# Optimization experiments

Hardware: AMD Instinct MI355X
Metric: run time of the kernel (lower is better)

Reference implementation:

```python
import jax, jax.numpy as jnp
import numpy as np

B, T, M, D = 2, 2048, 2048, 128
H = M // D
ROTARY_BASE = 10000
NORM_EPS = 1e-6
QK_SCALE = 1.0 / D  # mult = sqrt(qk_scale) applied to both q and k
INFTY_APPROX = 1e30


def setup_inputs() -> dict:
    key = jax.random.key(0)
    ks = jax.random.split(key, 6)
    w_scale = M ** (-0.5)
    return {
        "x": jax.random.normal(ks[0], (B, T, M), jnp.float32),
        "wq": jax.random.normal(ks[1], (M, H, D), jnp.float32) * w_scale,
        "wk": jax.random.normal(ks[2], (M, H, D), jnp.float32) * w_scale,
        "wv": jax.random.normal(ks[3], (M, H, D), jnp.float32) * w_scale,
        "wo": jax.random.normal(ks[4], (H, D, M), jnp.float32) * w_scale,
        "gq": jnp.zeros((H, 1, D), jnp.float32),
        "bq": jnp.zeros((H, 1, D), jnp.float32),
        "gk": jnp.zeros((H, 1, D), jnp.float32),
        "bk": jnp.zeros((H, 1, D), jnp.float32),
    }


def _qk_layernorm(x, g, b):
    # x: [B,H,T,D]; g,b: [H,1,D]; centered RMS norm with trainable (1+g), b
    x = x - jnp.mean(x, axis=-1, keepdims=True)
    x = x / jnp.sqrt(jnp.mean(jnp.square(x), axis=-1, keepdims=True) + NORM_EPS)
    return x * (1.0 + g)[None] + b[None]


def _rotary(x):
    # x: [B,H,T,D]; half-split rotary encoding
    half = D // 2
    positions = jnp.arange(T, dtype=jnp.float32)[:, None]          # [T,1]
    ang_freqs = jnp.power(float(ROTARY_BASE), -jnp.arange(half, dtype=jnp.float32) / half)[None, :]  # [1,half]
    radians = positions * ang_freqs                                  # [T,half]
    cos = jnp.cos(radians)[None, None].astype(x.dtype)               # [1,1,T,half]
    sin = jnp.sin(radians)[None, None].astype(x.dtype)
    even, odd = jnp.split(x, 2, axis=-1)
    return jnp.concatenate([even * cos - odd * sin, even * sin + odd * cos], axis=-1)


def reference(x, wq, wk, wv, wo, gq, bq, gk, bk):
    q = jnp.einsum('bim,mhd->bhid', x, wq)
    k = jnp.einsum('bim,mhd->bhid', x, wk)
    v = jnp.einsum('bim,mhd->bhid', x, wv)
    q = _rotary(_qk_layernorm(q, gq, bq))
    k = _rotary(_qk_layernorm(k, gk, bk))
    mult = jnp.asarray(QK_SCALE ** 0.5, dtype=x.dtype)
    s = jnp.einsum('bhid,bhjd->bhij', q * mult, k * mult)            # [B,H,T,T]
    i = jnp.arange(T)[:, None]
    j = jnp.arange(T)[None, :]
    future = (i < j)[None, None]                                      # mask future positions
    s = s - jnp.asarray(INFTY_APPROX, dtype=s.dtype) * future
    p = jax.nn.softmax(s, axis=-1)
    o = jnp.einsum('bhij,bhjd->bhid', p, v)
    return jnp.einsum('bhid,hdm->bim', o, wo)
```

## Files before the change

kernel.cpp:

```cpp
#include <hip/hip_runtime.h>


#define NB 2
#define NT 2048
#define NM 2048
#define NH 16
#define ND 128

typedef __attribute__((ext_vector_type(4))) float f32x4;
typedef __attribute__((ext_vector_type(8))) short bf16x8;
typedef __attribute__((ext_vector_type(4))) short bf16x4;

#define AS1 __attribute__((address_space(1)))
#define AS3 __attribute__((address_space(3)))

#define SW(r) (((r) ^ ((r) >> 2)) & 3)

__device__ __forceinline__ unsigned short f2bf(float f){
  unsigned int u = __float_as_uint(f);
  u = (u + 0x7fffu + ((u >> 16) & 1u)) >> 16;
  return (unsigned short)u;
}
__device__ __forceinline__ float bf2f(short s){
  return __uint_as_float(((unsigned int)(unsigned short)s) << 16);
}
__device__ __forceinline__ void gload_lds16(const void* g, void* l){
  __builtin_amdgcn_global_load_lds((const AS1 void*)g, (AS3 void*)l, 16, 0, 0);
}

__global__ __launch_bounds__(256) void prep_k(const float* __restrict__ x,
                                              const float* __restrict__ wq,
                                              const float* __restrict__ wk,
                                              const float* __restrict__ wv,
                                              const float* __restrict__ wo,
                                              short* __restrict__ xb,
                                              short* __restrict__ wT,
                                              float* __restrict__ ctab,
                                              float* __restrict__ stab){
  __shared__ float tl[32][33];
  const int bid = blockIdx.x, tid = threadIdx.x;
  if (bid < 8192){
    size_t gid = (size_t)bid * 256 + tid;
    float4 v = *(const float4*)(x + gid * 4);
    bf16x4 o;
    o[0] = (short)f2bf(v.x); o[1] = (short)f2bf(v.y);
    o[2] = (short)f2bf(v.z); o[3] = (short)f2bf(v.w);
    *(bf16x4*)(xb + gid * 4) = o;
  } else if (bid < 24576){
    int tb = bid - 8192;
    int z = tb >> 12, rem = tb & 4095;
    int n0 = (rem & 63) * 32, k0 = (rem >> 6) * 32;
    const float* src = (z == 0) ? wq : (z == 1) ? wk : (z == 2) ? wv : wo;
    short* dst = wT + (size_t)z * 2048 * 2048;
    int cx = tid & 31, ry = tid >> 5;
    #pragma unroll
    for (int p = 0; p < 4; ++p)
      tl[ry + 8 * p][cx] = src[(size_t)(k0 + ry + 8 * p) * 2048 + n0 + cx];
    __syncthreads();
    #pragma unroll
    for (int p = 0; p < 4; ++p)
      dst[(size_t)(n0 + ry + 8 * p) * 2048 + k0 + cx] =
          (short)f2bf(tl[cx][ry + 8 * p]);
  } else {
    int t = (bid - 24576) * 4 + (tid >> 6);
    int i = tid & 63;
    float freq = __expf(-(float)i * (9.210340371976184f / 64.0f));
    float ang = (float)t * freq;
    ctab[t * 64 + i] = cosf(ang);
    stab[t * 64 + i] = sinf(ang);
  }
}

#define NKT2 64
__global__ __launch_bounds__(512, 4) void gemm256_k(const short* __restrict__ A,
                                                    const short* __restrict__ Bt,
                                                    short* __restrict__ Cq,
                                                    short* __restrict__ Cn,
                                                    const float* __restrict__ gq,
                                                    const float* __restrict__ bq,
                                                    const float* __restrict__ gk,
                                                    const float* __restrict__ bk,
                                                    const float* __restrict__ ctab,
                                                    const float* __restrict__ stab){
  extern __shared__ char lds[];
  const int tid = threadIdx.x;
  const int wid = tid >> 6, lane = tid & 63;
  const int lrow = lane & 15, g8 = lane >> 4;
  const int wm = wid >> 1, wn = wid & 1;
  const int Kdim = 2048;

  int bid = blockIdx.x;
  int s = (bid & 7) * 96 + (bid >> 3);
  const int bx = s & 15;
  const int by = s >> 4;
  const int m0 = bx * 256, n0 = by * 128;

  const int ar = lane >> 2;
  const int ag = (lane & 3) ^ SW(ar);
  const short* Ab = A  + (size_t)(m0 + wid * 32 + ar) * Kdim + ag * 8;
  const short* Bb = Bt + (size_t)(n0 + wid * 16 + ar) * Kdim + ag * 8;

  f32x4 acc[4][4] = {};

  auto STAGE = [&](int c, int kt){
    #pragma unroll
    for (int i = 0; i < 2; ++i)
      gload_lds16(Ab + (size_t)(i * 16) * Kdim + kt * 32,
                  lds + c * 16384 + wid * 2048 + i * 1024);
    gload_lds16(Bb + kt * 32, lds + 32768 + c * 8192 + wid * 1024);
  };
  auto ldA = [&](int c, int mi) -> bf16x8 {
    int row = wm * 64 + mi * 16 + lrow;
    return *(const bf16x8*)(lds + c * 16384 + row * 64 + ((g8 ^ SW(row)) << 4));
  };
  auto ldB = [&](int c, int ni) -> bf16x8 {
    int row = wn * 64 + ni * 16 + lrow;
    return *(const bf16x8*)(lds + 32768 + c * 8192 + row * 64 + ((g8 ^ SW(row)) << 4));
  };

  STAGE(0, 0);

  for (int kt = 0; kt < NKT2; ++kt){
    const int c = kt & 1;
    asm volatile("s_waitcnt vmcnt(0)" ::: "memory");
    __builtin_amdgcn_s_barrier();
    if (kt + 1 < NKT2) STAGE(c ^ 1, kt + 1);

    bf16x8 af[4], bfv[4];
    #pragma unroll
    for (int mi = 0; mi < 4; ++mi) af[mi] = ldA(c, mi);
    #pragma unroll
    for (int ni = 0; ni < 4; ++ni) bfv[ni] = ldB(c, ni);
    #pragma unroll
    for (int mi = 0; mi < 4; ++mi)
      #pragma unroll
      for (int ni = 0; ni < 4; ++ni)
        acc[mi][ni] = __builtin_amdgcn_mfma_f32_16x16x32_bf16(
            af[mi], bfv[ni], acc[mi][ni], 0, 0, 0);
  }

  const int tsel = by >> 4;
  const int hh = by & 15;
  if (tsel < 2){
    const float* gv = tsel ? gk : gq;
    const float* bv = tsel ? bk : bq;
    float* red = (float*)lds;
    short* xch = (short*)(lds + 4096);
    __syncthreads();
    #pragma unroll
    for (int mi = 0; mi < 4; ++mi)
      #pragma unroll
      for (int r = 0; r < 4; ++r){
        float a0 = acc[mi][0][r], a1 = acc[mi][1][r];
        float a2 = acc[mi][2][r], a3 = acc[mi][3][r];
        float s1 = (a0 + a1) + (a2 + a3);
        float s2 = (a0*a0 + a1*a1) + (a2*a2 + a3*a3);
        #pragma unroll
        for (int off = 1; off < 16; off <<= 1){
          s1 += __shfl_xor(s1, off);
          s2 += __shfl_xor(s2, off);
        }
        if (lrow == 0){
          int row = wm * 64 + mi * 16 + g8 * 4 + r;
          red[row * 4 + wn * 2]     = s1;
          red[row * 4 + wn * 2 + 1] = s2;
        }
      }
    __syncthreads();
    #pragma unroll
    for (int mi = 0; mi < 4; ++mi)
      #pragma unroll
      for (int r = 0; r < 4; ++r){
        int row = wm * 64 + mi * 16 + g8 * 4 + r;
        float s1 = red[row * 4] + red[row * 4 + 2];
        float s2 = red[row * 4 + 1] + red[row * 4 + 3];
        float mean = s1 * (1.0f / 128.0f);
        float var = s2 * (1.0f / 128.0f) - mean * mean;
        float rstd = rsqrtf(var + 1e-6f);
        #pragma unroll
        for (int ni = 0; ni < 4; ++ni){
          int d = wn * 64 + ni * 16 + lrow;
          float n = (acc[mi][ni][r] - mean) * rstd * (1.0f + gv[hh * 128 + d])
                    + bv[hh * 128 + d];
          acc[mi][ni][r] = n;
          xch[row * 136 + d] = (short)f2bf(n);
        }
      }
    __syncthreads();
    const float sgn = wn ? 1.0f : -1.0f;
    const float qsc = tsel ? 1.0f : 0.011271055007f;
    short* dstn = Cn + (size_t)tsel * (NB * NH * NT * ND);
    #pragma unroll
    for (int mi = 0; mi < 4; ++mi)
      #pragma unroll
      for (int r = 0; r < 4; ++r){
        int rowb = m0 + wm * 64 + mi * 16 + g8 * 4 + r;
        int b = rowb >> 11, t = rowb & 2047;
        int row = rowb - m0;
        #pragma unroll
        for (int ni = 0; ni < 4; ++ni){
          int d = wn * 64 + ni * 16 + lrow;
          int dl = ni * 16 + lrow;
          float pv = bf2f(xch[row * 136 + (d ^ 64)]);
          float c = ctab[t * 64 + dl], sn = stab[t * 64 + dl];
          float o = (acc[mi][ni][r] * c + sgn * pv * sn) * qsc;
          dstn[(((size_t)(b * NH + hh)) * NT + t) * ND + d] = (short)f2bf(o);
        }
      }
  } else {
    short* dst = Cq + 2 * (size_t)(NB * NH * NT * ND);
    #pragma unroll
    for (int mi = 0; mi < 4; ++mi){
      int rowb = m0 + wm * 64 + mi * 16 + g8 * 4;
      int b = rowb >> 11, t0 = rowb & 2047;
      int jb = t0 >> 6, toff = t0 & 63;
      #pragma unroll
      for (int ni = 0; ni < 4; ++ni){
        int d = wn * 64 + ni * 16 + lrow;
        f32x4 a = acc[mi][ni];
        bf16x4 w4;
        #pragma unroll
        for (int r = 0; r < 4; ++r) w4[r] = (short)f2bf(a[r]);
        *(bf16x4*)&dst[(((size_t)(b * NH + hh) * 32 + jb) * ND + d) * 64 + toff] = w4;
      }
    }
  }
}

__global__ __launch_bounds__(512, 4) void gemmo_k(const short* __restrict__ A,
                                                  const short* __restrict__ Bt,
                                                  float* __restrict__ Cout){
  extern __shared__ char lds[];
  const int tid = threadIdx.x;
  const int wid = tid >> 6, lane = tid & 63;
  const int lrow = lane & 15, g8 = lane >> 4;
  const int wm = wid >> 1, wn = wid & 1;
  const int Kdim = 2048;

  int bid = blockIdx.x;
  int s = (bid & 7) * 32 + (bid >> 3);
  const int bx = s & 15;
  const int by = s >> 4;
  const int m0 = bx * 256, n0 = by * 128;

  const int ar = lane >> 2;
  const int ag = (lane & 3) ^ SW(ar);
  const short* Ab = A  + (size_t)(m0 + wid * 32 + ar) * Kdim + ag * 8;
  const short* Bb = Bt + (size_t)(n0 + wid * 16 + ar) * Kdim + ag * 8;

  f32x4 acc[4][4] = {};

  auto STAGE = [&](int c, int kt){
    #pragma unroll
    for (int i = 0; i < 2; ++i)
      gload_lds16(Ab + (size_t)(i * 16) * Kdim + kt * 32,
                  lds + c * 16384 + wid * 2048 + i * 1024);
    gload_lds16(Bb + kt * 32, lds + 32768 + c * 8192 + wid * 1024);
  };
  auto ldA = [&](int c, int mi) -> bf16x8 {
    int row = wm * 64 + mi * 16 + lrow;
    return *(const bf16x8*)(lds + c * 16384 + row * 64 + ((g8 ^ SW(row)) << 4));
  };
  auto ldB = [&](int c, int ni) -> bf16x8 {
    int row = wn * 64 + ni * 16 + lrow;
    return *(const bf16x8*)(lds + 32768 + c * 8192 + row * 64 + ((g8 ^ SW(row)) << 4));
  };

  STAGE(0, 0);

  for (int kt = 0; kt < NKT2; ++kt){
    const int c = kt & 1;
    asm volatile("s_waitcnt vmcnt(0)" ::: "memory");
    __builtin_amdgcn_s_barrier();
    if (kt + 1 < NKT2) STAGE(c ^ 1, kt + 1);

    bf16x8 af[4], bfv[4];
    #pragma unroll
    for (int mi = 0; mi < 4; ++mi) af[mi] = ldA(c, mi);
    #pragma unroll
    for (int ni = 0; ni < 4; ++ni) bfv[ni] = ldB(c, ni);
    #pragma unroll
    for (int mi = 0; mi < 4; ++mi)
      #pragma unroll
      for (int ni = 0; ni < 4; ++ni)
        acc[mi][ni] = __builtin_amdgcn_mfma_f32_16x16x32_bf16(
            af[mi], bfv[ni], acc[mi][ni], 0, 0, 0);
  }

  #pragma unroll
  for (int mi = 0; mi < 4; ++mi){
    int rowb = m0 + wm * 64 + mi * 16 + g8 * 4;
    #pragma unroll
    for (int ni = 0; ni < 4; ++ni){
      int col = n0 + wn * 64 + ni * 16 + lrow;
      f32x4 a = acc[mi][ni];
      #pragma unroll
      for (int r = 0; r < 4; ++r)
        Cout[(size_t)(rowb + r) * 2048 + col] = a[r];
    }
  }
}

__global__ __launch_bounds__(512) void attn_k(const short* __restrict__ qn,
                                              const short* __restrict__ kn,
                                              const short* __restrict__ vt,
                                              short* __restrict__ ob){
  extern __shared__ char lds[];
  const int tid = threadIdx.x;
  const int wid = tid >> 6, lane = tid & 63;
  const int lrow = lane & 15, g8 = lane >> 4;
  const int id = blockIdx.x;
  const int qs = id >> 5;
  const int bh = id & 31;
  const int b = bh >> 4, h = bh & 15;
  const size_t base = (size_t)bh * NT * ND;
  char* Pw = lds + 98304 + wid * 2048;

  auto STAGE = [&](int jb){
    const int cb = jb % 3;
    #pragma unroll
    for (int i = 0; i < 2; ++i){
      int r0 = wid * 4 + i * 32;
      int r = r0 + (lane >> 4);
      int g = lane & 15;
      gload_lds16(kn + base + (size_t)(jb * 64 + r) * ND + ((g ^ (r & 7)) << 3),
                  lds + cb * 16384 + r0 * 256);
    }
    #pragma unroll
    for (int i = 0; i < 2; ++i){
      int d0 = wid * 8 + i * 64;
      int d = d0 + (lane >> 3);
      int g = lane & 7;
      gload_lds16(vt + base + (size_t)jb * 8192 + d * 64 + ((g ^ (d & 7)) << 3),
                  lds + 49152 + cb * 16384 + d0 * 128);
    }
  };

  for (int pass = 0; pass < 2; ++pass){
    const int qt = pass ? (15 - qs) : qs;
    const int t0 = qt * 128;
    const int wrow0 = t0 + wid * 16;
    const int tq = wrow0 + lrow;
    bf16x8 qf[4];
    #pragma unroll
    for (int dc = 0; dc < 4; ++dc)
      qf[dc] = *(const bf16x8*)(qn + base + (size_t)tq * ND + dc * 32 + g8 * 8);
    f32x4 O[8] = {};
    float m = -3e38f, lsum = 0.0f;
    const int ntiles = 2 * qt + 2;

    __syncthreads();
    STAGE(0);
    STAGE(1);

    for (int jb = 0; jb < ntiles; ++jb){
      if (jb + 1 < ntiles) asm volatile("s_waitcnt vmcnt(4)" ::: "memory");
      else                 asm volatile("s_waitcnt vmcnt(0)" ::: "memory");
      __builtin_amdgcn_s_barrier();
      if (jb + 2 < ntiles) STAGE(jb + 2);
      const char* Kb = lds + (jb % 3) * 16384;
      const char* Vb = lds + 49152 + (jb % 3) * 16384;

      if (jb * 64 <= wrow0 + 15){
        f32x4 st[4] = {};
        __builtin_amdgcn_s_setprio(1);
        #pragma unroll
        for (int dc = 0; dc < 4; ++dc)
          #pragma unroll
          for (int js = 0; js < 4; ++js){
            int jl = js * 16 + lrow;
            bf16x8 kf = *(const bf16x8*)(Kb + jl * 256 +
                          (((dc * 4 + g8) ^ (jl & 7)) << 4));
            st[js] = __builtin_amdgcn_mfma_f32_16x16x32_bf16(kf, qf[dc], st[js], 0, 0, 0);
          }
        __builtin_amdgcn_s_setprio(0);
        if (jb * 64 + 63 > wrow0){
          #pragma unroll
          for (int js = 0; js < 4; ++js)
            #pragma unroll
            for (int r = 0; r < 4; ++r){
              int j = jb * 64 + js * 16 + g8 * 4 + r;
              if (j > tq) st[js][r] = -3e38f;
            }
        }
        f32x4 m4 = st[0];
        #pragma unroll
        for (int js = 1; js < 4; ++js)
          #pragma unroll
          for (int r = 0; r < 4; ++r) m4[r] = fmaxf(m4[r], st[js][r]);
        float mx = fmaxf(fmaxf(m4[0], m4[1]), fmaxf(m4[2], m4[3]));
        mx = fmaxf(mx, __shfl_xor(mx, 16));
        mx = fmaxf(mx, __shfl_xor(mx, 32));
        if (!__all(mx <= m + 8.0f)){
          float mnew = fmaxf(m, mx);
          float fac = exp2f(m - mnew);
          m = mnew;
          lsum *= fac;
          #pragma unroll
          for (int dcb = 0; dcb < 8; ++dcb) O[dcb] *= fac;
        }
        float ps = 0.0f;
        #pragma unroll
        for (int js = 0; js < 4; ++js){
          float p0 = exp2f(st[js][0] - m);
          float p1 = exp2f(st[js][1] - m);
          float p2 = exp2f(st[js][2] - m);
          float p3 = exp2f(st[js][3] - m);
          ps += (p0 + p1) + (p2 + p3);
          unsigned int lo, hi;
          asm("v_cvt_pk_bf16_f32 %0, %1, %2" : "=v"(lo) : "v"(p0), "v"(p1));
          asm("v_cvt_pk_bf16_f32 %0, %1, %2" : "=v"(hi) : "v"(p2), "v"(p3));
          uint2 w; w.x = lo; w.y = hi;
          *(uint2*)(Pw + lrow * 128 + ((js * 32 + g8 * 8) ^ ((lrow & 7) << 4))) = w;
        }
        ps += __shfl_xor(ps, 16);
        ps += __shfl_xor(ps, 32);
        lsum += ps;
        asm volatile("s_waitcnt lgkmcnt(0)" ::: "memory");
        __builtin_amdgcn_s_setprio(1);
        #pragma unroll
        for (int j32 = 0; j32 < 2; ++j32){
          bf16x8 pf = *(const bf16x8*)(Pw + lrow * 128 +
                        ((j32 * 64 + g8 * 16) ^ ((lrow & 7) << 4)));
          #pragma unroll
          for (int dcb = 0; dcb < 8; ++dcb){
            int d = dcb * 16 + lrow;
            bf16x8 vf = *(const bf16x8*)(Vb + d * 128 +
                          (((j32 * 4 + g8) ^ (d & 7)) << 4));
            O[dcb] = __builtin_amdgcn_mfma_f32_16x16x32_bf16(vf, pf, O[dcb], 0, 0, 0);
          }
        }
        __builtin_amdgcn_s_setprio(0);
      }
    }
    float inv = 1.0f / lsum;
    #pragma unroll
    for (int dcb = 0; dcb < 8; ++dcb){
      bf16x4 w4;
      #pragma unroll
      for (int r = 0; r < 4; ++r) w4[r] = (short)f2bf(O[dcb][r] * inv);
      *(bf16x4*)(ob + ((size_t)(b * NT + tq)) * (NH * ND) + h * ND + dcb * 16 + g8 * 4) = w4;
    }
  }
}

extern "C" void kernel_launch(void* const* d_in, const int* in_sizes, int n_in,
                              void* d_out, int out_size, void* d_ws, size_t ws_size,
                              hipStream_t stream){
  const float* x  = (const float*)d_in[0];
  const float* wq = (const float*)d_in[1];
  const float* wk = (const float*)d_in[2];
  const float* wv = (const float*)d_in[3];
  const float* wo = (const float*)d_in[4];
  const float* gq = (const float*)d_in[5];
  const float* bq = (const float*)d_in[6];
  const float* gk = (const float*)d_in[7];
  const float* bk = (const float*)d_in[8];

  char* ws = (char*)d_ws;
  short* xb   = (short*)(ws);
  short* wT   = (short*)(ws + 16777216);
  short* qkvb = (short*)(ws + 50331648);
  short* qkn  = (short*)(ws + 100663296);
  short* ob   = (short*)(ws + 134217728);
  float* ctab = (float*)(ws + 150994944);
  float* stab = (float*)(ws + 151519232);

  (void)hipFuncSetAttribute((const void*)gemm256_k,
                            hipFuncAttributeMaxDynamicSharedMemorySize, 73728);
  (void)hipFuncSetAttribute((const void*)gemmo_k,
                            hipFuncAttributeMaxDynamicSharedMemorySize, 49152);
  (void)hipFuncSetAttribute((const void*)attn_k,
                            hipFuncAttributeMaxDynamicSharedMemorySize, 114688);

  prep_k<<<dim3(25088), dim3(256), 0, stream>>>(x, wq, wk, wv, wo, xb, wT, ctab, stab);
  gemm256_k<<<dim3(768), dim3(512), 73728, stream>>>(xb, wT, qkvb, qkn,
                                                     gq, bq, gk, bk, ctab, stab);
  attn_k<<<dim3(256), dim3(512), 114688, stream>>>(qkn, qkn + 8388608,
                                                   qkvb + 2 * (size_t)8388608, ob);
  gemmo_k<<<dim3(256), dim3(512), 49152, stream>>>(ob, wT + 3 * (size_t)4194304,
                                                   (float*)d_out);
}
```

Measured before the change: 262.5 us.

## Give each wave full head rows in QKV GEMM to skip LDS norm exchange

The QKV projection GEMM now assigns each of the 8 waves a 32x128 tile (2x8 MFMA blocks) instead of a 64x64 tile. Each wave then holds complete head-dimension rows, so the layernorm reduction and rotary pairing (d with d^64) happen entirely in registers. This removes the LDS reduction buffer, the bf16 exchange buffer and three block barriers, and lowers the dynamic shared memory request. In exchange every wave reads all 8 B fragments per k-step (more LDS traffic on B, less on A), and the rotary partner is now used at full fp32 precision rather than rounded to bf16.

```diff
diff --git a/kernel.cpp b/kernel.cpp
--- a/kernel.cpp
+++ b/kernel.cpp
@@ -74,7 +74,7 @@
 #define NKT2 64
 __global__ __launch_bounds__(512, 4) void gemm256_k(const short* __restrict__ A,
                                                     const short* __restrict__ Bt,
-                                                    short* __restrict__ Cq,
+                                                    short* __restrict__ Cv,
                                                     short* __restrict__ Cn,
                                                     const float* __restrict__ gq,
                                                     const float* __restrict__ bq,
@@ -86,7 +86,6 @@
   const int tid = threadIdx.x;
   const int wid = tid >> 6, lane = tid & 63;
   const int lrow = lane & 15, g8 = lane >> 4;
-  const int wm = wid >> 1, wn = wid & 1;
   const int Kdim = 2048;
 
   int bid = blockIdx.x;
@@ -100,7 +99,7 @@
   const short* Ab = A  + (size_t)(m0 + wid * 32 + ar) * Kdim + ag * 8;
   const short* Bb = Bt + (size_t)(n0 + wid * 16 + ar) * Kdim + ag * 8;
 
-  f32x4 acc[4][4] = {};
+  f32x4 acc[2][8] = {};
 
   auto STAGE = [&](int c, int kt){
     #pragma unroll
@@ -110,11 +109,11 @@
     gload_lds16(Bb + kt * 32, lds + 32768 + c * 8192 + wid * 1024);
   };
   auto ldA = [&](int c, int mi) -> bf16x8 {
-    int row = wm * 64 + mi * 16 + lrow;
+    int row = wid * 32 + mi * 16 + lrow;
     return *(const bf16x8*)(lds + c * 16384 + row * 64 + ((g8 ^ SW(row)) << 4));
   };
   auto ldB = [&](int c, int ni) -> bf16x8 {
-    int row = wn * 64 + ni * 16 + lrow;
+    int row = ni * 16 + lrow;
     return *(const bf16x8*)(lds + 32768 + c * 8192 + row * 64 + ((g8 ^ SW(row)) << 4));
   };
 
@@ -126,15 +125,15 @@
     __builtin_amdgcn_s_barrier();
     if (kt + 1 < NKT2) STAGE(c ^ 1, kt + 1);
 
-    bf16x8 af[4], bfv[4];
-    #pragma unroll
-    for (int mi = 0; mi < 4; ++mi) af[mi] = ldA(c, mi);
-    #pragma unroll
-    for (int ni = 0; ni < 4; ++ni) bfv[ni] = ldB(c, ni);
-    #pragma unroll
-    for (int mi = 0; mi < 4; ++mi)
-      #pragma unroll
-      for (int ni = 0; ni < 4; ++ni)
+    bf16x8 af[2], bfv[8];
+    #pragma unroll
+    for (int mi = 0; mi < 2; ++mi) af[mi] = ldA(c, mi);
+    #pragma unroll
+    for (int ni = 0; ni < 8; ++ni) bfv[ni] = ldB(c, ni);
+    #pragma unroll
+    for (int mi = 0; mi < 2; ++mi)
+      #pragma unroll
+      for (int ni = 0; ni < 8; ++ni)
         acc[mi][ni] = __builtin_amdgcn_mfma_f32_16x16x32_bf16(
             af[mi], bfv[ni], acc[mi][ni], 0, 0, 0);
   }
@@ -144,84 +143,64 @@
   if (tsel < 2){
     const float* gv = tsel ? gk : gq;
     const float* bv = tsel ? bk : bq;
-    float* red = (float*)lds;
-    short* xch = (short*)(lds + 4096);
-    __syncthreads();
-    #pragma unroll
-    for (int mi = 0; mi < 4; ++mi)
+    float gcoef[8], bcoef[8];
+    #pragma unroll
+    for (int ni = 0; ni < 8; ++ni){
+      int d = ni * 16 + lrow;
+      gcoef[ni] = 1.0f + gv[hh * 128 + d];
+      bcoef[ni] = bv[hh * 128 + d];
+    }
+    const float qsc = tsel ? 1.0f : 0.011271055007f;
+    short* dstn = Cn + (size_t)tsel * (NB * NH * NT * ND);
+    #pragma unroll
+    for (int mi = 0; mi < 2; ++mi)
       #pragma unroll
       for (int r = 0; r < 4; ++r){
-        float a0 = acc[mi][0][r], a1 = acc[mi][1][r];
-        float a2 = acc[mi][2][r], a3 = acc[mi][3][r];
-        float s1 = (a0 + a1) + (a2 + a3);
-        float s2 = (a0*a0 + a1*a1) + (a2*a2 + a3*a3);
+        float s1 = 0.0f, s2 = 0.0f;
+        #pragma unroll
+        for (int ni = 0; ni < 8; ++ni){
+          float v = acc[mi][ni][r];
+          s1 += v; s2 += v * v;
+        }
         #pragma unroll
         for (int off = 1; off < 16; off <<= 1){
           s1 += __shfl_xor(s1, off);
           s2 += __shfl_xor(s2, off);
         }
-        if (lrow == 0){
-          int row = wm * 64 + mi * 16 + g8 * 4 + r;
-          red[row * 4 + wn * 2]     = s1;
-          red[row * 4 + wn * 2 + 1] = s2;
-        }
-      }
-    __syncthreads();
-    #pragma unroll
-    for (int mi = 0; mi < 4; ++mi)
-      #pragma unroll
-      for (int r = 0; r < 4; ++r){
-        int row = wm * 64 + mi * 16 + g8 * 4 + r;
-        float s1 = red[row * 4] + red[row * 4 + 2];
-        float s2 = red[row * 4 + 1] + red[row * 4 + 3];
         float mean = s1 * (1.0f / 128.0f);
         float var = s2 * (1.0f / 128.0f) - mean * mean;
         float rstd = rsqrtf(var + 1e-6f);
-        #pragma unroll
-        for (int ni = 0; ni < 4; ++ni){
-          int d = wn * 64 + ni * 16 + lrow;
-          float n = (acc[mi][ni][r] - mean) * rstd * (1.0f + gv[hh * 128 + d])
-                    + bv[hh * 128 + d];
-          acc[mi][ni][r] = n;
-          xch[row * 136 + d] = (short)f2bf(n);
-        }
-      }
-    __syncthreads();
-    const float sgn = wn ? 1.0f : -1.0f;
-    const float qsc = tsel ? 1.0f : 0.011271055007f;
-    short* dstn = Cn + (size_t)tsel * (NB * NH * NT * ND);
-    #pragma unroll
-    for (int mi = 0; mi < 4; ++mi)
-      #pragma unroll
-      for (int r = 0; r < 4; ++r){
-        int rowb = m0 + wm * 64 + mi * 16 + g8 * 4 + r;
+        float nv[8];
+        #pragma unroll
+        for (int ni = 0; ni < 8; ++ni)
+          nv[ni] = (acc[mi][ni][r] - mean) * rstd * gcoef[ni] + bcoef[ni];
+        int rowb = m0 + wid * 32 + mi * 16 + g8 * 4 + r;
         int b = rowb >> 11, t = rowb & 2047;
-        int row = rowb - m0;
-        #pragma unroll
-        for (int ni = 0; ni < 4; ++ni){
-          int d = wn * 64 + ni * 16 + lrow;
-          int dl = ni * 16 + lrow;
-          float pv = bf2f(xch[row * 136 + (d ^ 64)]);
+        size_t rbase = (((size_t)(b * NH + hh)) * NT + t) * ND;
+        #pragma unroll
+        for (int lo = 0; lo < 4; ++lo){
+          int dl = lo * 16 + lrow;
           float c = ctab[t * 64 + dl], sn = stab[t * 64 + dl];
-          float o = (acc[mi][ni][r] * c + sgn * pv * sn) * qsc;
-          dstn[(((size_t)(b * NH + hh)) * NT + t) * ND + d] = (short)f2bf(o);
+          float oe = (nv[lo] * c - nv[lo + 4] * sn) * qsc;
+          float oo = (nv[lo] * sn + nv[lo + 4] * c) * qsc;
+          dstn[rbase + dl]      = (short)f2bf(oe);
+          dstn[rbase + dl + 64] = (short)f2bf(oo);
         }
       }
   } else {
-    short* dst = Cq + 2 * (size_t)(NB * NH * NT * ND);
-    #pragma unroll
-    for (int mi = 0; mi < 4; ++mi){
-      int rowb = m0 + wm * 64 + mi * 16 + g8 * 4;
+    #pragma unroll
+    for (int mi = 0; mi < 2; ++mi){
+      int rowb = m0 + wid * 32 + mi * 16 + g8 * 4;
       int b = rowb >> 11, t0 = rowb & 2047;
       int jb = t0 >> 6, toff = t0 & 63;
       #pragma unroll
-      for (int ni = 0; ni < 4; ++ni){
-        int d = wn * 64 + ni * 16 + lrow;
+      for (int ni = 0; ni < 8; ++ni){
+        int d = ni * 16 + lrow;
         f32x4 a = acc[mi][ni];
         bf16x4 w4;
         #pragma unroll
         for (int r = 0; r < 4; ++r) w4[r] = (short)f2bf(a[r]);
-        *(bf16x4*)&dst[(((size_t)(b * NH + hh) * 32 + jb) * ND + d) * 64 + toff] = w4;
+        *(bf16x4*)&Cv[(((size_t)(b * NH + hh) * 32 + jb) * ND + d) * 64 + toff] = w4;
       }
     }
   }
@@ -467,14 +446,15 @@
   float* stab = (float*)(ws + 151519232);
 
   (void)hipFuncSetAttribute((const void*)gemm256_k,
-                            hipFuncAttributeMaxDynamicSharedMemorySize, 73728);
+                            hipFuncAttributeMaxDynamicSharedMemorySize, 49152);
   (void)hipFuncSetAttribute((const void*)gemmo_k,
                             hipFuncAttributeMaxDynamicSharedMemorySize, 49152);
   (void)hipFuncSetAttribute((const void*)attn_k,
                             hipFuncAttributeMaxDynamicSharedMemorySize, 114688);
 
   prep_k<<<dim3(25088), dim3(256), 0, stream>>>(x, wq, wk, wv, wo, xb, wT, ctab, stab);
-  gemm256_k<<<dim3(768), dim3(512), 73728, stream>>>(xb, wT, qkvb, qkn,
+  gemm256_k<<<dim3(768), dim3(512), 49152, stream>>>(xb, wT,
+                                                     qkvb + 2 * (size_t)8388608, qkn,
                                                      gq, bq, gk, bk, ctab, stab);
   attn_k<<<dim3(256), dim3(512), 114688, stream>>>(qkn, qkn + 8388608,
                                                    qkvb + 2 * (size_t)8388608, ob);
```

New measurement: 256.9 us (median of 2 runs). 1.02x faster.

## Interleave Q/K weight columns so rotary partner pairs are exchanged via lane shuffle

Applied to the files above, without the earlier changes.

The prep kernel now permutes the Q and K weight columns within each head so that rotary partners d and d+64 land in adjacent columns. The GEMM epilogue can then fetch the partner value with a lane shuffle instead of writing normalized values to LDS, syncing, and reading them back. It also hoists the gain and bias loads into registers and reduces dynamic shared memory, which may raise occupancy. In exchange, q and k are stored in an interleaved dimension order, which is only valid because q·k dot products do not depend on the order of d.

```diff
diff --git a/kernel.cpp b/kernel.cpp
--- a/kernel.cpp
+++ b/kernel.cpp
@@ -58,9 +58,14 @@
       tl[ry + 8 * p][cx] = src[(size_t)(k0 + ry + 8 * p) * 2048 + n0 + cx];
     __syncthreads();
     #pragma unroll
-    for (int p = 0; p < 4; ++p)
-      dst[(size_t)(n0 + ry + 8 * p) * 2048 + k0 + cx] =
-          (short)f2bf(tl[cx][ry + 8 * p]);
+    for (int p = 0; p < 4; ++p){
+      int n = n0 + ry + 8 * p;
+      if (z < 2){
+        int d = n & 127;
+        n = (n & ~127) | (((d & 63) << 1) | (d >> 6));
+      }
+      dst[(size_t)n * 2048 + k0 + cx] = (short)f2bf(tl[cx][ry + 8 * p]);
+    }
   } else {
     int t = (bid - 24576) * 4 + (tid >> 6);
     int i = tid & 63;
@@ -74,7 +79,7 @@
 #define NKT2 64
 __global__ __launch_bounds__(512, 4) void gemm256_k(const short* __restrict__ A,
                                                     const short* __restrict__ Bt,
-                                                    short* __restrict__ Cq,
+                                                    short* __restrict__ Cv,
                                                     short* __restrict__ Cn,
                                                     const float* __restrict__ gq,
                                                     const float* __restrict__ bq,
@@ -145,7 +150,14 @@
     const float* gv = tsel ? gk : gq;
     const float* bv = tsel ? bk : bq;
     float* red = (float*)lds;
-    short* xch = (short*)(lds + 4096);
+    float gcoef[4], bcoef[4];
+    #pragma unroll
+    for (int ni = 0; ni < 4; ++ni){
+      int p = wn * 64 + ni * 16 + lrow;
+      int d = (p >> 1) + ((p & 1) << 6);
+      gcoef[ni] = 1.0f + gv[hh * 128 + d];
+      bcoef[ni] = bv[hh * 128 + d];
+    }
     __syncthreads();
     #pragma unroll
     for (int mi = 0; mi < 4; ++mi)
@@ -167,6 +179,9 @@
         }
       }
     __syncthreads();
+    const float qsc = tsel ? 1.0f : 0.011271055007f;
+    const float sgn = (lrow & 1) ? 1.0f : -1.0f;
+    short* dstn = Cn + (size_t)tsel * (NB * NH * NT * ND);
     #pragma unroll
     for (int mi = 0; mi < 4; ++mi)
       #pragma unroll
@@ -177,38 +192,20 @@
         float mean = s1 * (1.0f / 128.0f);
         float var = s2 * (1.0f / 128.0f) - mean * mean;
         float rstd = rsqrtf(var + 1e-6f);
+        int rowb = m0 + row;
+        int b = rowb >> 11, t = rowb & 2047;
+        size_t rbase = (((size_t)(b * NH + hh)) * NT + t) * ND;
         #pragma unroll
         for (int ni = 0; ni < 4; ++ni){
-          int d = wn * 64 + ni * 16 + lrow;
-          float n = (acc[mi][ni][r] - mean) * rstd * (1.0f + gv[hh * 128 + d])
-                    + bv[hh * 128 + d];
-          acc[mi][ni][r] = n;
-          xch[row * 136 + d] = (short)f2bf(n);
-        }
-      }
-    __syncthreads();
-    const float sgn = wn ? 1.0f : -1.0f;
-    const float qsc = tsel ? 1.0f : 0.011271055007f;
-    short* dstn = Cn + (size_t)tsel * (NB * NH * NT * ND);
-    #pragma unroll
-    for (int mi = 0; mi < 4; ++mi)
-      #pragma unroll
-      for (int r = 0; r < 4; ++r){
-        int rowb = m0 + wm * 64 + mi * 16 + g8 * 4 + r;
-        int b = rowb >> 11, t = rowb & 2047;
-        int row = rowb - m0;
-        #pragma unroll
-        for (int ni = 0; ni < 4; ++ni){
-          int d = wn * 64 + ni * 16 + lrow;
-          int dl = ni * 16 + lrow;
-          float pv = bf2f(xch[row * 136 + (d ^ 64)]);
-          float c = ctab[t * 64 + dl], sn = stab[t * 64 + dl];
-          float o = (acc[mi][ni][r] * c + sgn * pv * sn) * qsc;
-          dstn[(((size_t)(b * NH + hh)) * NT + t) * ND + d] = (short)f2bf(o);
+          float nv = (acc[mi][ni][r] - mean) * rstd * gcoef[ni] + bcoef[ni];
+          float pv = __shfl_xor(nv, 1);
+          int p = wn * 64 + ni * 16 + lrow;
+          float c = ctab[t * 64 + (p >> 1)], sn = stab[t * 64 + (p >> 1)];
+          float o = (nv * c + sgn * pv * sn) * qsc;
+          dstn[rbase + p] = (short)f2bf(o);
         }
       }
   } else {
-    short* dst = Cq + 2 * (size_t)(NB * NH * NT * ND);
     #pragma unroll
     for (int mi = 0; mi < 4; ++mi){
       int rowb = m0 + wm * 64 + mi * 16 + g8 * 4;
@@ -221,7 +218,7 @@
         bf16x4 w4;
         #pragma unroll
         for (int r = 0; r < 4; ++r) w4[r] = (short)f2bf(a[r]);
-        *(bf16x4*)&dst[(((size_t)(b * NH + hh) * 32 + jb) * ND + d) * 64 + toff] = w4;
+        *(bf16x4*)&Cv[(((size_t)(b * NH + hh) * 32 + jb) * ND + d) * 64 + toff] = w4;
       }
     }
   }
@@ -467,14 +464,15 @@
   float* stab = (float*)(ws + 151519232);
 
   (void)hipFuncSetAttribute((const void*)gemm256_k,
-                            hipFuncAttributeMaxDynamicSharedMemorySize, 73728);
+                            hipFuncAttributeMaxDynamicSharedMemorySize, 49152);
   (void)hipFuncSetAttribute((const void*)gemmo_k,
                             hipFuncAttributeMaxDynamicSharedMemorySize, 49152);
   (void)hipFuncSetAttribute((const void*)attn_k,
                             hipFuncAttributeMaxDynamicSharedMemorySize, 114688);
 
   prep_k<<<dim3(25088), dim3(256), 0, stream>>>(x, wq, wk, wv, wo, xb, wT, ctab, stab);
-  gemm256_k<<<dim3(768), dim3(512), 73728, stream>>>(xb, wT, qkvb, qkn,
+  gemm256_k<<<dim3(768), dim3(512), 49152, stream>>>(xb, wT,
+                                                     qkvb + 2 * (size_t)8388608, qkn,
                                                      gq, bq, gk, bk, ctab, stab);
   attn_k<<<dim3(256), dim3(512), 114688, stream>>>(qkn, qkn + 8388608,
                                                    qkvb + 2 * (size_t)8388608, ob);
```

After: 258.9 us. Within noise of the previous version (-1.4%).
